# Performance work log

Measured on AMD Instinct MI355X. Metric: run time of the kernel, lower is better.

## Reference

```python
import jax, jax.numpy as jnp
import numpy as np
from jax import lax

B, CIN, S = 16, 1, 64          # batch, input channels, spatial
C = 16                          # c_out hidden channels
T = 50                          # ODE steps
DT = 0.5
NC = 7                          # n_classes
K = T // 2 + 1                  # rfft bins = 26
HID = 256


def conv2d_same(x, w, b):
    # x:(B,Ci,H,W) w:(Co,Ci,3,3) zero 'SAME' padding (torch padding=1)
    y = lax.conv_general_dilated(x, w, (1, 1), 'SAME',
                                 dimension_numbers=('NCHW', 'OIHW', 'NCHW'))
    return y + b[None, :, None, None]


def conv2d_circular(x, w):
    # circular padding=1, no bias (coRNNCell.Wy)
    xp = jnp.pad(x, ((0, 0), (0, 0), (1, 1), (1, 1)), mode='wrap')
    return lax.conv_general_dilated(xp, w, (1, 1), 'VALID',
                                    dimension_numbers=('NCHW', 'OIHW', 'NCHW'))


def setup_inputs() -> dict:
    key = jax.random.key(0)
    ks = iter(jax.random.split(key, 40))
    d = {}
    d['x'] = jax.random.normal(next(ks), (B, CIN, S, S), dtype=jnp.float32)

    def cw(ci, co):
        return jax.random.normal(next(ks), (co, ci, 3, 3), jnp.float32) * (1.0 / np.sqrt(ci * 9))

    # omega / alpha encoders: 3 convs each
    for p in ('om', 'al'):
        d[f'{p}_w1'], d[f'{p}_b1'] = cw(CIN, C), jnp.zeros((C,), jnp.float32)
        d[f'{p}_w2'], d[f'{p}_b2'] = cw(C, C), jnp.zeros((C,), jnp.float32)
        d[f'{p}_w3'], d[f'{p}_b3'] = cw(C, C), jnp.zeros((C,), jnp.float32)
    # hy encoder: 4 convs
    d['hy_w1'], d['hy_b1'] = cw(CIN, C), jnp.zeros((C,), jnp.float32)
    d['hy_w2'], d['hy_b2'] = cw(C, C), jnp.zeros((C,), jnp.float32)
    d['hy_w3'], d['hy_b3'] = cw(C, C), jnp.zeros((C,), jnp.float32)
    d['hy_w4'], d['hy_b4'] = cw(C, C), jnp.zeros((C,), jnp.float32)
    # cell conv: block-diagonal discrete Laplacian (per torch init)
    lap = np.array([[0., 1., 0.], [1., -4., 1.], [0., 1., 0.]], np.float32)
    wy = np.zeros((C, C, 3, 3), np.float32)
    wy[np.arange(C), np.arange(C)] = lap
    d['wy'] = jnp.asarray(wy)
    # readout MLP: 416 -> 256 -> 256 -> 256 -> 7
    dims = [K * C, HID, HID, HID, NC]
    for i in range(4):
        d[f'ro_w{i+1}'] = jax.random.normal(next(ks), (dims[i], dims[i + 1]), jnp.float32) * (1.0 / np.sqrt(dims[i]))
        d[f'ro_b{i+1}'] = jnp.zeros((dims[i + 1],), jnp.float32)
    return d


def _forward(x,
             om_w1, om_b1, om_w2, om_b2, om_w3, om_b3,
             al_w1, al_b1, al_w2, al_b2, al_w3, al_b3,
             hy_w1, hy_b1, hy_w2, hy_b2, hy_w3, hy_b3, hy_w4, hy_b4,
             wy,
             ro_w1, ro_b1, ro_w2, ro_b2, ro_w3, ro_b3, ro_w4, ro_b4):
    relu = jax.nn.relu
    # encoders
    om = relu(conv2d_same(relu(conv2d_same(relu(conv2d_same(x, om_w1, om_b1)), om_w2, om_b2)), om_w3, om_b3))
    al = relu(conv2d_same(relu(conv2d_same(relu(conv2d_same(x, al_w1, al_b1)), al_w2, al_b2)), al_w3, al_b3))
    h = relu(conv2d_same(x, hy_w1, hy_b1))
    h = relu(conv2d_same(h, hy_w2, hy_b2))
    h = relu(conv2d_same(h, hy_w3, hy_b3))
    hy0 = jnp.tanh(conv2d_same(h, hy_w4, hy_b4))

    omega = om.reshape(B, C, S * S)
    alpha = al.reshape(B, C, S * S)
    hy = hy0.reshape(B, C, S * S)
    hz = jnp.zeros_like(hy)

    def step(carry, _):
        hy, hz = carry
        sf = jnp.tanh(conv2d_circular(hy.reshape(B, C, S, S), wy)).reshape(B, C, S * S)
        new_hz = hz + DT * (sf - omega * hy - alpha * hz)
        new_hy = hy + DT * new_hz
        return (new_hy, new_hz), new_hy

    _, y_seq = lax.scan(step, (hy, hz), None, length=T)   # (T,B,C,HW)
    y_seq = jnp.transpose(y_seq, (1, 3, 2, 0)).reshape(B * S * S, C, T)  # (BHW,C,T)

    fft_mag = jnp.abs(jnp.fft.rfft(y_seq, axis=2))        # (BHW,C,K)
    f = fft_mag.reshape(B * S * S, C * K)                  # (BHW, C*K)

    f = relu(f @ ro_w1 + ro_b1)
    f = relu(f @ ro_w2 + ro_b2)
    f = relu(f @ ro_w3 + ro_b3)
    logits_flat = f @ ro_w4 + ro_b4                        # (BHW, NC)
    logits = logits_flat.reshape(B, S, S, NC).transpose(0, 3, 1, 2)
    return logits


def reference(x,
              om_w1, om_b1, om_w2, om_b2, om_w3, om_b3,
              al_w1, al_b1, al_w2, al_b2, al_w3, al_b3,
              hy_w1, hy_b1, hy_w2, hy_b2, hy_w3, hy_b3, hy_w4, hy_b4,
              wy,
              ro_w1, ro_b1, ro_w2, ro_b2, ro_w3, ro_b3, ro_w4, ro_b4):
    return _forward(x,
                    om_w1, om_b1, om_w2, om_b2, om_w3, om_b3,
                    al_w1, al_b1, al_w2, al_b2, al_w3, al_b3,
                    hy_w1, hy_b1, hy_w2, hy_b2, hy_w3, hy_b3, hy_w4, hy_b4,
                    wy,
                    ro_w1, ro_b1, ro_w2, ro_b2, ro_w3, ro_b3, ro_w4, ro_b4)
```

## Files before the change

### kernel.cpp

```cpp
#include <hip/hip_runtime.h>
#include <hip/hip_bf16.h>
#include <hip/hip_fp16.h>
#include <math.h>

#define B_   16
#define C_   16
#define S_   64
#define HW_  4096
#define T_   50
#define K_   26
#define F_   416
#define HID_ 256
#define NC_  7
#define DT_  0.5f
#define BCHW_ (B_*C_*HW_)
#define M_   (B_*HW_)

typedef short    bf16x8 __attribute__((ext_vector_type(8)));
typedef _Float16 f16x8  __attribute__((ext_vector_type(8)));
typedef float    f32x4  __attribute__((ext_vector_type(4)));

__device__ __forceinline__ void gld_lds16(const void* g, void* l){
    __builtin_amdgcn_global_load_lds(
        (const __attribute__((address_space(1))) void*)g,
        (__attribute__((address_space(3))) void*)l, 16, 0, 0);
}

__device__ __forceinline__ float fast_tanh(float x){
    float ax = fabsf(x);
    float e  = __expf(2.f*ax);
    float r  = 1.f - 2.f/(e + 1.f);
    return copysignf(r, x);
}

__device__ __forceinline__ float b2f(short s){
    return __uint_as_float(((unsigned int)(unsigned short)s) << 16);
}
__device__ __forceinline__ short f2b(float f){
    __hip_bfloat16 h = __float2bfloat16(f);
    return *(short*)&h;
}

template<int CIN, int ACT>
__global__ __launch_bounds__(1024) void convf_kernel(
    const float* __restrict__ in0, const float* __restrict__ in1, const float* __restrict__ in2,
    const float* __restrict__ w0,  const float* __restrict__ w1,  const float* __restrict__ w2,
    const float* __restrict__ b0,  const float* __restrict__ b1,  const float* __restrict__ b2,
    float* __restrict__ o0, float* __restrict__ o1, float* __restrict__ o2)
{
    __shared__ float slab[CIN][18][66];
    const int slice = blockIdx.x;
    const int b     = blockIdx.y;
    const int ch    = blockIdx.z;
    const float* in = (ch == 0) ? in0 : (ch == 1) ? in1 : in2;
    const float* w  = (ch == 0) ? w0  : (ch == 1) ? w1  : w2;
    const float* bb = (ch == 0) ? b0  : (ch == 1) ? b1  : b2;
    float* out      = (ch == 0) ? o0  : (ch == 1) ? o1  : o2;

    const int tid = threadIdx.x;
    const int y0  = slice * 16;

    for (int idx = tid; idx < CIN*18*66; idx += 1024){
        int ci  = idx / (18*66);
        int rem = idx % (18*66);
        int rr  = rem / 66;
        int cc  = rem % 66;
        int gy = y0 - 1 + rr;
        int gx = cc - 1;
        float v = 0.f;
        if ((unsigned)gy < 64u && (unsigned)gx < 64u)
            v = in[(size_t)(b*CIN + ci)*HW_ + gy*64 + gx];
        slab[ci][rr][cc] = v;
    }
    __syncthreads();

    const int x  = tid & 63;
    const int ry = tid >> 6;

    float acc[16];
    #pragma unroll
    for (int co = 0; co < 16; co++) acc[co] = bb[co];

    for (int ci = 0; ci < CIN; ci++){
        float p[3][3];
        #pragma unroll
        for (int dy = 0; dy < 3; dy++)
            #pragma unroll
            for (int dx = 0; dx < 3; dx++)
                p[dy][dx] = slab[ci][ry + dy][x + dx];
        #pragma unroll
        for (int co = 0; co < 16; co++){
            const float* wp = w + (size_t)(co*CIN + ci)*9;
            float s = acc[co];
            #pragma unroll
            for (int dy = 0; dy < 3; dy++)
                #pragma unroll
                for (int dx = 0; dx < 3; dx++)
                    s = fmaf(wp[dy*3 + dx], p[dy][dx], s);
            acc[co] = s;
        }
    }
    #pragma unroll
    for (int co = 0; co < 16; co++){
        float v = acc[co];
        v = ACT ? fast_tanh(v) : fmaxf(v, 0.f);
        out[(size_t)(b*16 + co)*HW_ + (y0 + ry)*64 + x] = v;
    }
}

__global__ __launch_bounds__(1024) void ode_kernel(
    const float* __restrict__ omega, const float* __restrict__ alpha,
    const float* __restrict__ hy0,   const float* __restrict__ wy,
    __half* __restrict__ yseq)
{
    __shared__ float buf[2][64*65];
    const int blk = blockIdx.x;
    const int c   = blk & 15;
    const int tid = threadIdx.x;
    const int x   = tid & 63;
    const int sy  = (tid >> 6) << 2;
    const size_t off = (size_t)blk * HW_;

    float om[4], al[4], hz[4], hy[4];
    #pragma unroll
    for (int i = 0; i < 4; i++){
        size_t g = off + (size_t)(sy + i)*64 + x;
        om[i] = omega[g];
        al[i] = alpha[g];
        hz[i] = 0.f;
        hy[i] = hy0[g];
        buf[0][x*65 + sy + i] = hy[i];
    }
    float wv[9];
    const float* wp = wy + (size_t)(c*C_ + c)*9;
    #pragma unroll
    for (int j = 0; j < 9; j++) wv[j] = wp[j];
    const bool five = (wv[0]==0.f) & (wv[2]==0.f) & (wv[6]==0.f) & (wv[8]==0.f);
    __syncthreads();

    const int xl = ((x + 63) & 63) * 65;
    const int xr = ((x + 1)  & 63) * 65;
    const int xo = x * 65;
    const int ylo = (sy + 63) & 63;
    const int yhi = (sy + 4)  & 63;

    int cur = 0;
    for (int t = 0; t < T_; t++){
        const float* hp = buf[cur];
        float* hn = buf[cur ^ 1];
        float l[6], r[6];
        #pragma unroll
        for (int i = 0; i < 4; i++){ l[i+1] = hp[xl + sy + i]; r[i+1] = hp[xr + sy + i]; }
        if (!five){
            l[0] = hp[xl + ylo];  r[0] = hp[xr + ylo];
            l[5] = hp[xl + yhi];  r[5] = hp[xr + yhi];
        }
        float tN = hp[xo + ylo];
        float tS = hp[xo + yhi];

        __half* yout = yseq + (size_t)t*BCHW_ + off;
        float ny[4];
        #pragma unroll
        for (int i = 0; i < 4; i++){
            float up = (i == 0) ? tN : hy[i-1];
            float dn = (i == 3) ? tS : hy[i+1];
            float s = wv[1]*up + wv[3]*l[i+1] + wv[4]*hy[i] + wv[5]*r[i+1] + wv[7]*dn;
            if (!five)
                s += wv[0]*l[i] + wv[2]*r[i] + wv[6]*l[i+2] + wv[8]*r[i+2];
            float sf = fast_tanh(s);
            float nz = hz[i] + DT_*(sf - om[i]*hy[i] - al[i]*hz[i]);
            float v  = hy[i] + DT_*nz;
            hz[i] = nz;
            ny[i] = v;
        }
        #pragma unroll
        for (int i = 0; i < 4; i++){
            hy[i] = ny[i];
            hn[xo + sy + i] = ny[i];
            yout[(sy + i)*64 + x] = __float2half(ny[i]);
        }
        __syncthreads();
        cur ^= 1;
    }
}

__global__ __launch_bounds__(256) void dft_mfma_kernel(
    const __half* __restrict__ yseq, __hip_bfloat16* __restrict__ f)
{
    __shared__ char Ys[8*256*16];
    __shared__ char Gs[8*64*16];
    const int tid = threadIdx.x;
    const int blk = blockIdx.x;
    const int bc  = blk >> 4;
    const int p0  = (blk & 15) << 8;
    const int b   = bc >> 4, c = bc & 15;

    for (int idx = tid; idx < 64*64; idx += 256){
        int r = idx >> 6, t = idx & 63;
        float v = 0.f;
        if (r < 52 && t < 50){
            int k  = r >> 1;
            int ph = (k * t) % 50;
            float ang = (float)ph * (6.2831853071795864f / 50.f);
            v = (r & 1) ? sinf(ang) : cosf(ang);
        }
        *(_Float16*)(Gs + ((t >> 3)*64 + r)*16 + (t & 7)*2) = (_Float16)v;
    }

    {
        const __half* src = yseq + (size_t)bc*HW_ + p0 + tid;
        #pragma unroll
        for (int t2 = 0; t2 < 25; t2++){
            unsigned int a = *(const unsigned short*)&src[(size_t)(2*t2)*BCHW_];
            unsigned int d = *(const unsigned short*)&src[(size_t)(2*t2+1)*BCHW_];
            int t8 = t2 >> 2, j = t2 & 3;
            *(unsigned int*)(Ys + (t8*256 + tid)*16 + j*4) = a | (d << 16);
        }
        #pragma unroll
        for (int t2 = 25; t2 < 32; t2++){
            int t8 = t2 >> 2, j = t2 & 3;
            *(unsigned int*)(Ys + (t8*256 + tid)*16 + j*4) = 0u;
        }
    }
    __syncthreads();

    const int lane = tid & 63;
    const int w    = tid >> 6;
    const int n    = lane & 15;
    const int quad = lane >> 4;
    const int mrow = 16*w + n;

    f16x8 a0 = *(const f16x8*)(Gs + ((quad    )*64 + mrow)*16);
    f16x8 a1 = *(const f16x8*)(Gs + ((quad + 4)*64 + mrow)*16);

    const int kb0   = 8*w + 2*quad;
    const bool valid = (kb0 < K_);

    for (int nt = 0; nt < 16; nt++){
        f16x8 b0 = *(const f16x8*)(Ys + ((quad    )*256 + nt*16 + n)*16);
        f16x8 b1 = *(const f16x8*)(Ys + ((quad + 4)*256 + nt*16 + n)*16);
        f32x4 acc = (f32x4){0.f, 0.f, 0.f, 0.f};
        acc = __builtin_amdgcn_mfma_f32_16x16x32_f16(a0, b0, acc, 0, 0, 0);
        acc = __builtin_amdgcn_mfma_f32_16x16x32_f16(a1, b1, acc, 0, 0, 0);
        if (valid){
            float m0 = sqrtf(fmaf(acc[0], acc[0], acc[1]*acc[1]));
            float m1 = sqrtf(fmaf(acc[2], acc[2], acc[3]*acc[3]));
            unsigned int u = ((unsigned int)(unsigned short)f2b(m1) << 16)
                           |  (unsigned int)(unsigned short)f2b(m0);
            const int row = b*HW_ + p0 + nt*16 + n;
            *(unsigned int*)((char*)(f + (size_t)row*F_ + c*K_) + kb0*2) = u;
        }
    }
}

__global__ __launch_bounds__(256) void prep_wt_kernel(
    const float* __restrict__ w, __hip_bfloat16* __restrict__ wt, int Kd, int N)
{
    const int n = blockIdx.x;
    for (int k = threadIdx.x; k < Kd; k += 256)
        wt[(size_t)n*Kd + k] = __float2bfloat16(w[(size_t)k*N + n]);
}

__global__ __launch_bounds__(512, 2) void mlp_fused_kernel(
    const __hip_bfloat16* __restrict__ A,
    const __hip_bfloat16* __restrict__ Wt1,
    const __hip_bfloat16* __restrict__ Wt2,
    const __hip_bfloat16* __restrict__ Wt3,
    const float* __restrict__ b1, const float* __restrict__ b2,
    const float* __restrict__ b3,
    const float* __restrict__ w4, const float* __restrict__ b4,
    float* __restrict__ out)
{
    __shared__ short hbuf[256*258];
    __shared__ short Bs[1024*8];
    __shared__ float w4s[HID_*NC_];

    const int tid  = threadIdx.x;
    const int lane = tid & 63;
    const int wave = tid >> 6;
    const int wm   = (wave & 3) * 64;
    const int wn   = (wave >> 2) * 128;
    const int n16  = lane & 15;
    const int quad = lane >> 4;
    const int m0   = blockIdx.x * 256;

    for (int i = tid; i < HID_*NC_; i += 512) w4s[i] = w4[i];

    const int id0 = tid, id1 = tid + 512;
    const int kc0 = id0 >> 8, nn0 = id0 & 255;
    const int kc1 = id1 >> 8, nn1 = id1 & 255;

    f32x4 acc[4][8];
    #pragma unroll
    for (int i = 0; i < 4; i++)
        #pragma unroll
        for (int j = 0; j < 8; j++)
            acc[i][j] = (f32x4){0.f,0.f,0.f,0.f};

    const __hip_bfloat16* arow[4];
    #pragma unroll
    for (int i = 0; i < 4; i++)
        arow[i] = A + (size_t)(m0 + wm + i*16 + n16)*F_ + quad*8;

    bf16x8 afn[4];
    #pragma unroll
    for (int i = 0; i < 4; i++) afn[i] = *(const bf16x8*)(arow[i]);

    for (int k0 = 0; k0 < F_; k0 += 32){
        gld_lds16(Wt1 + (size_t)nn0*F_ + k0 + kc0*8, (char*)Bs + id0*16);
        gld_lds16(Wt1 + (size_t)nn1*F_ + k0 + kc1*8, (char*)Bs + id1*16);
        __syncthreads();
        bf16x8 af[4];
        #pragma unroll
        for (int i = 0; i < 4; i++) af[i] = afn[i];
        if (k0 + 32 < F_){
            #pragma unroll
            for (int i = 0; i < 4; i++) afn[i] = *(const bf16x8*)(arow[i] + k0 + 32);
        }
        bf16x8 bf[8];
        #pragma unroll
        for (int j = 0; j < 8; j++)
            bf[j] = *(const bf16x8*)&Bs[(quad*256 + wn + j*16 + n16)*8];
        #pragma unroll
        for (int i = 0; i < 4; i++)
            #pragma unroll
            for (int j = 0; j < 8; j++)
                acc[i][j] = __builtin_amdgcn_mfma_f32_16x16x32_bf16(
                                af[i], bf[j], acc[i][j], 0, 0, 0);
        __syncthreads();
    }
    #pragma unroll
    for (int j = 0; j < 8; j++){
        const int col = wn + j*16 + n16;
        const float bv = b1[col];
        #pragma unroll
        for (int i = 0; i < 4; i++){
            const int r0 = wm + i*16 + quad*4;
            #pragma unroll
            for (int r = 0; r < 4; r++)
                hbuf[(r0 + r)*258 + col] = f2b(fmaxf(acc[i][j][r] + bv, 0.f));
        }
    }
    __syncthreads();

    const __hip_bfloat16* Wts[2] = {Wt2, Wt3};
    const float* bls[2] = {b2, b3};
    for (int L = 0; L < 2; L++){
        const __hip_bfloat16* Wt = Wts[L];
        #pragma unroll
        for (int i = 0; i < 4; i++)
            #pragma unroll
            for (int j = 0; j < 8; j++)
                acc[i][j] = (f32x4){0.f,0.f,0.f,0.f};

        for (int k0 = 0; k0 < HID_; k0 += 32){
            gld_lds16(Wt + (size_t)nn0*HID_ + k0 + kc0*8, (char*)Bs + id0*16);
            gld_lds16(Wt + (size_t)nn1*HID_ + k0 + kc1*8, (char*)Bs + id1*16);
            bf16x8 af[4];
            #pragma unroll
            for (int i = 0; i < 4; i++)
                af[i] = *(const bf16x8*)&hbuf[(wm + i*16 + n16)*258 + k0 + quad*8];
            __syncthreads();
            bf16x8 bf[8];
            #pragma unroll
            for (int j = 0; j < 8; j++)
                bf[j] = *(const bf16x8*)&Bs[(quad*256 + wn + j*16 + n16)*8];
            #pragma unroll
            for (int i = 0; i < 4; i++)
                #pragma unroll
                for (int j = 0; j < 8; j++)
                    acc[i][j] = __builtin_amdgcn_mfma_f32_16x16x32_bf16(
                                    af[i], bf[j], acc[i][j], 0, 0, 0);
            __syncthreads();
        }
        const float* bl = bls[L];
        #pragma unroll
        for (int j = 0; j < 8; j++){
            const int col = wn + j*16 + n16;
            const float bv = bl[col];
            #pragma unroll
            for (int i = 0; i < 4; i++){
                const int r0 = wm + i*16 + quad*4;
                #pragma unroll
                for (int r = 0; r < 4; r++)
                    hbuf[(r0 + r)*258 + col] = f2b(fmaxf(acc[i][j][r] + bv, 0.f));
            }
        }
        __syncthreads();
    }

    const int row = tid >> 1;
    const int sel = tid & 1;
    const int j0  = sel ? 4 : 0;
    const int nj  = sel ? 3 : 4;

    float facc[4];
    #pragma unroll
    for (int t = 0; t < 4; t++) facc[t] = (t < nj) ? b4[j0 + t] : 0.f;

    for (int k8 = 0; k8 < HID_/8; k8++){
        bf16x8 hv = *(const bf16x8*)&hbuf[row*258 + k8*8];
        #pragma unroll
        for (int e = 0; e < 8; e++){
            float vv = b2f(hv[e]);
            const float* wr = &w4s[(k8*8 + e)*NC_ + j0];
            #pragma unroll
            for (int t = 0; t < 4; t++)
                if (t < nj) facc[t] = fmaf(vv, wr[t], facc[t]);
        }
    }
    const int grow = m0 + row;
    const int bidx = grow >> 12, hw = grow & 4095;
    #pragma unroll
    for (int t = 0; t < 4; t++)
        if (t < nj)
            out[(size_t)(bidx*NC_ + j0 + t)*HW_ + hw] = facc[t];
}

extern "C" void kernel_launch(void* const* d_in, const int* in_sizes, int n_in,
                              void* d_out, int out_size, void* d_ws, size_t ws_size,
                              hipStream_t stream)
{
    const float* x     = (const float*)d_in[0];
    const float* om_w1 = (const float*)d_in[1];  const float* om_b1 = (const float*)d_in[2];
    const float* om_w2 = (const float*)d_in[3];  const float* om_b2 = (const float*)d_in[4];
    const float* om_w3 = (const float*)d_in[5];  const float* om_b3 = (const float*)d_in[6];
    const float* al_w1 = (const float*)d_in[7];  const float* al_b1 = (const float*)d_in[8];
    const float* al_w2 = (const float*)d_in[9];  const float* al_b2 = (const float*)d_in[10];
    const float* al_w3 = (const float*)d_in[11]; const float* al_b3 = (const float*)d_in[12];
    const float* hy_w1 = (const float*)d_in[13]; const float* hy_b1 = (const float*)d_in[14];
    const float* hy_w2 = (const float*)d_in[15]; const float* hy_b2 = (const float*)d_in[16];
    const float* hy_w3 = (const float*)d_in[17]; const float* hy_b3 = (const float*)d_in[18];
    const float* hy_w4 = (const float*)d_in[19]; const float* hy_b4 = (const float*)d_in[20];
    const float* wy    = (const float*)d_in[21];
    const float* ro_w1 = (const float*)d_in[22]; const float* ro_b1 = (const float*)d_in[23];
    const float* ro_w2 = (const float*)d_in[24]; const float* ro_b2 = (const float*)d_in[25];
    const float* ro_w3 = (const float*)d_in[26]; const float* ro_b3 = (const float*)d_in[27];
    const float* ro_w4 = (const float*)d_in[28]; const float* ro_b4 = (const float*)d_in[29];
    float* out = (float*)d_out;

    char* wsb = (char*)d_ws;
    const size_t YSEQ_BYTES = (size_t)T_ * BCHW_ * 2;
    __half* yseq = (__half*)wsb;
    __hip_bfloat16* fbuf = (__hip_bfloat16*)(wsb + YSEQ_BYTES);

    const size_t MB4 = (size_t)BCHW_ * 4;
    float* om_t1 = (float*)(wsb + YSEQ_BYTES + 0*MB4);
    float* al_t1 = (float*)(wsb + YSEQ_BYTES + 1*MB4);
    float* hy_t1 = (float*)(wsb + YSEQ_BYTES + 2*MB4);
    float* om_t2 = (float*)(wsb + YSEQ_BYTES + 3*MB4);
    float* al_t2 = (float*)(wsb + YSEQ_BYTES + 4*MB4);
    float* hy_t2 = (float*)(wsb + YSEQ_BYTES + 5*MB4);
    float* omega = (float*)(wsb + YSEQ_BYTES + 6*MB4);
    float* alpha = (float*)(wsb + YSEQ_BYTES + 7*MB4);
    float* hy_t3 = (float*)(wsb + YSEQ_BYTES + 8*MB4);
    float* hy0   = (float*)(wsb + YSEQ_BYTES + 9*MB4);

    __hip_bfloat16* wt1 = (__hip_bfloat16*)(wsb + 0);
    __hip_bfloat16* wt2 = (__hip_bfloat16*)(wsb + 212992);
    __hip_bfloat16* wt3 = (__hip_bfloat16*)(wsb + 344064);

    convf_kernel<1,0><<<dim3(4,B_,3), 1024, 0, stream>>>(
        x, x, x, om_w1, al_w1, hy_w1, om_b1, al_b1, hy_b1, om_t1, al_t1, hy_t1);
    convf_kernel<16,0><<<dim3(4,B_,3), 1024, 0, stream>>>(
        om_t1, al_t1, hy_t1, om_w2, al_w2, hy_w2, om_b2, al_b2, hy_b2, om_t2, al_t2, hy_t2);
    convf_kernel<16,0><<<dim3(4,B_,3), 1024, 0, stream>>>(
        om_t2, al_t2, hy_t2, om_w3, al_w3, hy_w3, om_b3, al_b3, hy_b3, omega, alpha, hy_t3);
    convf_kernel<16,1><<<dim3(4,B_,1), 1024, 0, stream>>>(
        hy_t3, hy_t3, hy_t3, hy_w4, hy_w4, hy_w4, hy_b4, hy_b4, hy_b4, hy0, hy0, hy0);
    ode_kernel<<<256, 1024, 0, stream>>>(omega, alpha, hy0, wy, yseq);
    dft_mfma_kernel<<<4096, 256, 0, stream>>>(yseq, fbuf);
    prep_wt_kernel<<<256, 256, 0, stream>>>(ro_w1, wt1, F_,   HID_);
    prep_wt_kernel<<<256, 256, 0, stream>>>(ro_w2, wt2, HID_, HID_);
    prep_wt_kernel<<<256, 256, 0, stream>>>(ro_w3, wt3, HID_, HID_);
    mlp_fused_kernel<<<256, 512, 0, stream>>>(
        fbuf, wt1, wt2, wt3, ro_b1, ro_b2, ro_b3, ro_w4, ro_b4, out);
}
```

Measured before the change: 413.9 us.

## Switch MLP to fp16 MFMA, MFMA final layer, pad LDS, retile convs

Moves the DFT output and MLP weights from bf16 to fp16 and computes the final 256->7 readout layer with MFMA on an fp16 copy of w4 staged in LDS, replacing the scalar FMA loop. It also pads the LDS row strides for the B tile and hidden buffer to reduce bank conflicts, and merges the three weight-transpose launches into one. The conv kernels move to 8-row slices with 512 threads, doubling the block count, and the DFT table uses fast sin/cos intrinsics. fp16 has less range than bf16, so FFT magnitudes and activations could lose accuracy or overflow.

Result: faster. 379.3 us (-8.4%).

```diff
diff --git a/kernel.cpp b/kernel.cpp
--- a/kernel.cpp
+++ b/kernel.cpp
@@ -16,7 +16,6 @@
 #define BCHW_ (B_*C_*HW_)
 #define M_   (B_*HW_)
 
-typedef short    bf16x8 __attribute__((ext_vector_type(8)));
 typedef _Float16 f16x8  __attribute__((ext_vector_type(8)));
 typedef float    f32x4  __attribute__((ext_vector_type(4)));
 
@@ -33,22 +32,19 @@
     return copysignf(r, x);
 }
 
-__device__ __forceinline__ float b2f(short s){
-    return __uint_as_float(((unsigned int)(unsigned short)s) << 16);
-}
-__device__ __forceinline__ short f2b(float f){
-    __hip_bfloat16 h = __float2bfloat16(f);
+__device__ __forceinline__ short f2h_s(float f){
+    __half h = __float2half(f);
     return *(short*)&h;
 }
 
 template<int CIN, int ACT>
-__global__ __launch_bounds__(1024) void convf_kernel(
+__global__ __launch_bounds__(512) void convf_kernel(
     const float* __restrict__ in0, const float* __restrict__ in1, const float* __restrict__ in2,
     const float* __restrict__ w0,  const float* __restrict__ w1,  const float* __restrict__ w2,
     const float* __restrict__ b0,  const float* __restrict__ b1,  const float* __restrict__ b2,
     float* __restrict__ o0, float* __restrict__ o1, float* __restrict__ o2)
 {
-    __shared__ float slab[CIN][18][66];
+    __shared__ __align__(16) float slab[CIN][10][66];
     const int slice = blockIdx.x;
     const int b     = blockIdx.y;
     const int ch    = blockIdx.z;
@@ -58,11 +54,11 @@
     float* out      = (ch == 0) ? o0  : (ch == 1) ? o1  : o2;
 
     const int tid = threadIdx.x;
-    const int y0  = slice * 16;
-
-    for (int idx = tid; idx < CIN*18*66; idx += 1024){
-        int ci  = idx / (18*66);
-        int rem = idx % (18*66);
+    const int y0  = slice * 8;
+
+    for (int idx = tid; idx < CIN*10*66; idx += 512){
+        int ci  = idx / (10*66);
+        int rem = idx % (10*66);
         int rr  = rem / 66;
         int cc  = rem % 66;
         int gy = y0 - 1 + rr;
@@ -113,7 +109,7 @@
     const float* __restrict__ hy0,   const float* __restrict__ wy,
     __half* __restrict__ yseq)
 {
-    __shared__ float buf[2][64*65];
+    __shared__ __align__(16) float buf[2][64*65];
     const int blk = blockIdx.x;
     const int c   = blk & 15;
     const int tid = threadIdx.x;
@@ -185,10 +181,10 @@
 }
 
 __global__ __launch_bounds__(256) void dft_mfma_kernel(
-    const __half* __restrict__ yseq, __hip_bfloat16* __restrict__ f)
-{
-    __shared__ char Ys[8*256*16];
-    __shared__ char Gs[8*64*16];
+    const __half* __restrict__ yseq, __half* __restrict__ f)
+{
+    __shared__ __align__(16) char Ys[8*256*16];
+    __shared__ __align__(16) char Gs[8*64*16];
     const int tid = threadIdx.x;
     const int blk = blockIdx.x;
     const int bc  = blk >> 4;
@@ -202,7 +198,7 @@
             int k  = r >> 1;
             int ph = (k * t) % 50;
             float ang = (float)ph * (6.2831853071795864f / 50.f);
-            v = (r & 1) ? sinf(ang) : cosf(ang);
+            v = (r & 1) ? __sinf(ang) : __cosf(ang);
         }
         *(_Float16*)(Gs + ((t >> 3)*64 + r)*16 + (t & 7)*2) = (_Float16)v;
     }
@@ -245,35 +241,49 @@
         if (valid){
             float m0 = sqrtf(fmaf(acc[0], acc[0], acc[1]*acc[1]));
             float m1 = sqrtf(fmaf(acc[2], acc[2], acc[3]*acc[3]));
-            unsigned int u = ((unsigned int)(unsigned short)f2b(m1) << 16)
-                           |  (unsigned int)(unsigned short)f2b(m0);
+            unsigned int u = ((unsigned int)(unsigned short)f2h_s(m1) << 16)
+                           |  (unsigned int)(unsigned short)f2h_s(m0);
             const int row = b*HW_ + p0 + nt*16 + n;
             *(unsigned int*)((char*)(f + (size_t)row*F_ + c*K_) + kb0*2) = u;
         }
     }
 }
 
-__global__ __launch_bounds__(256) void prep_wt_kernel(
-    const float* __restrict__ w, __hip_bfloat16* __restrict__ wt, int Kd, int N)
-{
-    const int n = blockIdx.x;
-    for (int k = threadIdx.x; k < Kd; k += 256)
-        wt[(size_t)n*Kd + k] = __float2bfloat16(w[(size_t)k*N + n]);
+__global__ __launch_bounds__(256) void prep_all_kernel(
+    const float* __restrict__ w1, const float* __restrict__ w2,
+    const float* __restrict__ w3,
+    __half* __restrict__ wt1, __half* __restrict__ wt2, __half* __restrict__ wt3)
+{
+    const int blk = blockIdx.x;
+    const int tid = threadIdx.x;
+    if (blk < 256){
+        const int n = blk;
+        for (int k = tid; k < F_; k += 256)
+            wt1[(size_t)n*F_ + k] = __float2half(w1[(size_t)k*HID_ + n]);
+    } else if (blk < 512){
+        const int n = blk - 256;
+        for (int k = tid; k < HID_; k += 256)
+            wt2[(size_t)n*HID_ + k] = __float2half(w2[(size_t)k*HID_ + n]);
+    } else {
+        const int n = blk - 512;
+        for (int k = tid; k < HID_; k += 256)
+            wt3[(size_t)n*HID_ + k] = __float2half(w3[(size_t)k*HID_ + n]);
+    }
 }
 
 __global__ __launch_bounds__(512, 2) void mlp_fused_kernel(
-    const __hip_bfloat16* __restrict__ A,
-    const __hip_bfloat16* __restrict__ Wt1,
-    const __hip_bfloat16* __restrict__ Wt2,
-    const __hip_bfloat16* __restrict__ Wt3,
+    const __half* __restrict__ A,
+    const __half* __restrict__ Wt1,
+    const __half* __restrict__ Wt2,
+    const __half* __restrict__ Wt3,
     const float* __restrict__ b1, const float* __restrict__ b2,
     const float* __restrict__ b3,
     const float* __restrict__ w4, const float* __restrict__ b4,
     float* __restrict__ out)
 {
-    __shared__ short hbuf[256*258];
-    __shared__ short Bs[1024*8];
-    __shared__ float w4s[HID_*NC_];
+    __shared__ __align__(16) short hbuf[256*264];
+    __shared__ __align__(16) short Bs[4*2064];
+    __shared__ __align__(16) short Bs4[512*8];
 
     const int tid  = threadIdx.x;
     const int lane = tid & 63;
@@ -284,11 +294,23 @@
     const int quad = lane >> 4;
     const int m0   = blockIdx.x * 256;
 
-    for (int i = tid; i < HID_*NC_; i += 512) w4s[i] = w4[i];
+    {
+        const int ktq = tid >> 4, n = tid & 15;
+        short vals[8];
+        #pragma unroll
+        for (int e = 0; e < 8; e++){
+            const int k = ktq*8 + e;
+            vals[e] = f2h_s((n < NC_) ? w4[(size_t)k*NC_ + n] : 0.f);
+        }
+        #pragma unroll
+        for (int e = 0; e < 8; e++) Bs4[tid*8 + e] = vals[e];
+    }
 
     const int id0 = tid, id1 = tid + 512;
     const int kc0 = id0 >> 8, nn0 = id0 & 255;
     const int kc1 = id1 >> 8, nn1 = id1 & 255;
+    char* dst0 = (char*)Bs + kc0*4128 + nn0*16;
+    char* dst1 = (char*)Bs + kc1*4128 + nn1*16;
 
     f32x4 acc[4][8];
     #pragma unroll
@@ -297,35 +319,35 @@
         for (int j = 0; j < 8; j++)
             acc[i][j] = (f32x4){0.f,0.f,0.f,0.f};
 
-    const __hip_bfloat16* arow[4];
+    const __half* arow[4];
     #pragma unroll
     for (int i = 0; i < 4; i++)
         arow[i] = A + (size_t)(m0 + wm + i*16 + n16)*F_ + quad*8;
 
-    bf16x8 afn[4];
-    #pragma unroll
-    for (int i = 0; i < 4; i++) afn[i] = *(const bf16x8*)(arow[i]);
+    f16x8 afn[4];
+    #pragma unroll
+    for (int i = 0; i < 4; i++) afn[i] = *(const f16x8*)(arow[i]);
 
     for (int k0 = 0; k0 < F_; k0 += 32){
-        gld_lds16(Wt1 + (size_t)nn0*F_ + k0 + kc0*8, (char*)Bs + id0*16);
-        gld_lds16(Wt1 + (size_t)nn1*F_ + k0 + kc1*8, (char*)Bs + id1*16);
+        gld_lds16(Wt1 + (size_t)nn0*F_ + k0 + kc0*8, dst0);
+        gld_lds16(Wt1 + (size_t)nn1*F_ + k0 + kc1*8, dst1);
         __syncthreads();
-        bf16x8 af[4];
+        f16x8 af[4];
         #pragma unroll
         for (int i = 0; i < 4; i++) af[i] = afn[i];
         if (k0 + 32 < F_){
             #pragma unroll
-            for (int i = 0; i < 4; i++) afn[i] = *(const bf16x8*)(arow[i] + k0 + 32);
-        }
-        bf16x8 bf[8];
+            for (int i = 0; i < 4; i++) afn[i] = *(const f16x8*)(arow[i] + k0 + 32);
+        }
+        f16x8 bf[8];
         #pragma unroll
         for (int j = 0; j < 8; j++)
-            bf[j] = *(const bf16x8*)&Bs[(quad*256 + wn + j*16 + n16)*8];
+            bf[j] = *(const f16x8*)((char*)Bs + quad*4128 + (wn + j*16 + n16)*16);
         #pragma unroll
         for (int i = 0; i < 4; i++)
             #pragma unroll
             for (int j = 0; j < 8; j++)
-                acc[i][j] = __builtin_amdgcn_mfma_f32_16x16x32_bf16(
+                acc[i][j] = __builtin_amdgcn_mfma_f32_16x16x32_f16(
                                 af[i], bf[j], acc[i][j], 0, 0, 0);
         __syncthreads();
     }
@@ -338,15 +360,15 @@
             const int r0 = wm + i*16 + quad*4;
             #pragma unroll
             for (int r = 0; r < 4; r++)
-                hbuf[(r0 + r)*258 + col] = f2b(fmaxf(acc[i][j][r] + bv, 0.f));
+                hbuf[(r0 + r)*264 + col] = f2h_s(fmaxf(acc[i][j][r] + bv, 0.f));
         }
     }
     __syncthreads();
 
-    const __hip_bfloat16* Wts[2] = {Wt2, Wt3};
+    const __half* Wts[2] = {Wt2, Wt3};
     const float* bls[2] = {b2, b3};
     for (int L = 0; L < 2; L++){
-        const __hip_bfloat16* Wt = Wts[L];
+        const __half* Wt = Wts[L];
         #pragma unroll
         for (int i = 0; i < 4; i++)
             #pragma unroll
@@ -354,22 +376,22 @@
                 acc[i][j] = (f32x4){0.f,0.f,0.f,0.f};
 
         for (int k0 = 0; k0 < HID_; k0 += 32){
-            gld_lds16(Wt + (size_t)nn0*HID_ + k0 + kc0*8, (char*)Bs + id0*16);
-            gld_lds16(Wt + (size_t)nn1*HID_ + k0 + kc1*8, (char*)Bs + id1*16);
-            bf16x8 af[4];
+            gld_lds16(Wt + (size_t)nn0*HID_ + k0 + kc0*8, dst0);
+            gld_lds16(Wt + (size_t)nn1*HID_ + k0 + kc1*8, dst1);
+            f16x8 af[4];
             #pragma unroll
             for (int i = 0; i < 4; i++)
-                af[i] = *(const bf16x8*)&hbuf[(wm + i*16 + n16)*258 + k0 + quad*8];
+                af[i] = *(const f16x8*)&hbuf[(wm + i*16 + n16)*264 + k0 + quad*8];
             __syncthreads();
-            bf16x8 bf[8];
+            f16x8 bf[8];
             #pragma unroll
             for (int j = 0; j < 8; j++)
-                bf[j] = *(const bf16x8*)&Bs[(quad*256 + wn + j*16 + n16)*8];
+                bf[j] = *(const f16x8*)((char*)Bs + quad*4128 + (wn + j*16 + n16)*16);
             #pragma unroll
             for (int i = 0; i < 4; i++)
                 #pragma unroll
                 for (int j = 0; j < 8; j++)
-                    acc[i][j] = __builtin_amdgcn_mfma_f32_16x16x32_bf16(
+                    acc[i][j] = __builtin_amdgcn_mfma_f32_16x16x32_f16(
                                     af[i], bf[j], acc[i][j], 0, 0, 0);
             __syncthreads();
         }
@@ -383,38 +405,34 @@
                 const int r0 = wm + i*16 + quad*4;
                 #pragma unroll
                 for (int r = 0; r < 4; r++)
-                    hbuf[(r0 + r)*258 + col] = f2b(fmaxf(acc[i][j][r] + bv, 0.f));
+                    hbuf[(r0 + r)*264 + col] = f2h_s(fmaxf(acc[i][j][r] + bv, 0.f));
             }
         }
         __syncthreads();
     }
 
-    const int row = tid >> 1;
-    const int sel = tid & 1;
-    const int j0  = sel ? 4 : 0;
-    const int nj  = sel ? 3 : 4;
-
-    float facc[4];
-    #pragma unroll
-    for (int t = 0; t < 4; t++) facc[t] = (t < nj) ? b4[j0 + t] : 0.f;
-
-    for (int k8 = 0; k8 < HID_/8; k8++){
-        bf16x8 hv = *(const bf16x8*)&hbuf[row*258 + k8*8];
-        #pragma unroll
-        for (int e = 0; e < 8; e++){
-            float vv = b2f(hv[e]);
-            const float* wr = &w4s[(k8*8 + e)*NC_ + j0];
-            #pragma unroll
-            for (int t = 0; t < 4; t++)
-                if (t < nj) facc[t] = fmaf(vv, wr[t], facc[t]);
-        }
-    }
-    const int grow = m0 + row;
-    const int bidx = grow >> 12, hw = grow & 4095;
-    #pragma unroll
-    for (int t = 0; t < 4; t++)
-        if (t < nj)
-            out[(size_t)(bidx*NC_ + j0 + t)*HW_ + hw] = facc[t];
+    f32x4 facc[2] = {(f32x4){0.f,0.f,0.f,0.f}, (f32x4){0.f,0.f,0.f,0.f}};
+    #pragma unroll
+    for (int kt = 0; kt < 8; kt++){
+        f16x8 bfr = *(const f16x8*)&Bs4[((kt*4 + quad)*16 + n16)*8];
+        #pragma unroll
+        for (int mt = 0; mt < 2; mt++){
+            f16x8 af = *(const f16x8*)&hbuf[(wave*32 + mt*16 + n16)*264 + kt*32 + quad*8];
+            facc[mt] = __builtin_amdgcn_mfma_f32_16x16x32_f16(af, bfr, facc[mt], 0, 0, 0);
+        }
+    }
+    if (n16 < NC_){
+        const float bv = b4[n16];
+        #pragma unroll
+        for (int mt = 0; mt < 2; mt++){
+            #pragma unroll
+            for (int r = 0; r < 4; r++){
+                const int grow = m0 + wave*32 + mt*16 + quad*4 + r;
+                const int bidx = grow >> 12, hw = grow & 4095;
+                out[(size_t)(bidx*NC_ + n16)*HW_ + hw] = facc[mt][r] + bv;
+            }
+        }
+    }
 }
 
 extern "C" void kernel_launch(void* const* d_in, const int* in_sizes, int n_in,
@@ -442,7 +460,7 @@
     char* wsb = (char*)d_ws;
     const size_t YSEQ_BYTES = (size_t)T_ * BCHW_ * 2;
     __half* yseq = (__half*)wsb;
-    __hip_bfloat16* fbuf = (__hip_bfloat16*)(wsb + YSEQ_BYTES);
+    __half* fbuf = (__half*)(wsb + YSEQ_BYTES);
 
     const size_t MB4 = (size_t)BCHW_ * 4;
     float* om_t1 = (float*)(wsb + YSEQ_BYTES + 0*MB4);
@@ -456,23 +474,21 @@
     float* hy_t3 = (float*)(wsb + YSEQ_BYTES + 8*MB4);
     float* hy0   = (float*)(wsb + YSEQ_BYTES + 9*MB4);
 
-    __hip_bfloat16* wt1 = (__hip_bfloat16*)(wsb + 0);
-    __hip_bfloat16* wt2 = (__hip_bfloat16*)(wsb + 212992);
-    __hip_bfloat16* wt3 = (__hip_bfloat16*)(wsb + 344064);
-
-    convf_kernel<1,0><<<dim3(4,B_,3), 1024, 0, stream>>>(
+    __half* wt1 = (__half*)(wsb + 0);
+    __half* wt2 = (__half*)(wsb + 212992);
+    __half* wt3 = (__half*)(wsb + 344064);
+
+    convf_kernel<1,0><<<dim3(8,B_,3), 512, 0, stream>>>(
         x, x, x, om_w1, al_w1, hy_w1, om_b1, al_b1, hy_b1, om_t1, al_t1, hy_t1);
-    convf_kernel<16,0><<<dim3(4,B_,3), 1024, 0, stream>>>(
+    convf_kernel<16,0><<<dim3(8,B_,3), 512, 0, stream>>>(
         om_t1, al_t1, hy_t1, om_w2, al_w2, hy_w2, om_b2, al_b2, hy_b2, om_t2, al_t2, hy_t2);
-    convf_kernel<16,0><<<dim3(4,B_,3), 1024, 0, stream>>>(
+    convf_kernel<16,0><<<dim3(8,B_,3), 512, 0, stream>>>(
         om_t2, al_t2, hy_t2, om_w3, al_w3, hy_w3, om_b3, al_b3, hy_b3, omega, alpha, hy_t3);
-    convf_kernel<16,1><<<dim3(4,B_,1), 1024, 0, stream>>>(
+    convf_kernel<16,1><<<dim3(8,B_,1), 512, 0, stream>>>(
         hy_t3, hy_t3, hy_t3, hy_w4, hy_w4, hy_w4, hy_b4, hy_b4, hy_b4, hy0, hy0, hy0);
     ode_kernel<<<256, 1024, 0, stream>>>(omega, alpha, hy0, wy, yseq);
     dft_mfma_kernel<<<4096, 256, 0, stream>>>(yseq, fbuf);
-    prep_wt_kernel<<<256, 256, 0, stream>>>(ro_w1, wt1, F_,   HID_);
-    prep_wt_kernel<<<256, 256, 0, stream>>>(ro_w2, wt2, HID_, HID_);
-    prep_wt_kernel<<<256, 256, 0, stream>>>(ro_w3, wt3, HID_, HID_);
+    prep_all_kernel<<<768, 256, 0, stream>>>(ro_w1, ro_w2, ro_w3, wt1, wt2, wt3);
     mlp_fused_kernel<<<256, 512, 0, stream>>>(
         fbuf, wt1, wt2, wt3, ro_b1, ro_b2, ro_b3, ro_w4, ro_b4, out);
 }
```
